# Kernel tuning notes

Hardware: AMD Instinct MI355X
Metric: run time of the kernel (lower is better)

## Reference

```python
import jax, jax.numpy as jnp
import numpy as np

B_, CIN, HH, WW = 2, 64, 64, 64
D_MODEL, D_INNER, D_STATE, DT_RANK, D_CONV = 64, 128, 16, 32, 3


def setup_inputs() -> dict:
    key = jax.random.key(0)
    ks = jax.random.split(key, 16)
    w = lambda k, shape: jax.random.normal(k, shape, jnp.float32) * 0.05
    # dt_proj bias init (torch: inv-softplus of dt sampled in [dt_min, dt_max])
    dt = jnp.exp(jax.random.uniform(ks[10], (D_INNER,)) * (np.log(0.1) - np.log(0.001)) + np.log(0.001))
    dt = jnp.clip(dt, 1e-4, None)
    inv_dt = dt + jnp.log(-jnp.expm1(-dt))
    A = jnp.tile(jnp.arange(1, D_STATE + 1, dtype=jnp.float32), (D_INNER, 1))
    return {
        "rgb_feat": jax.random.normal(ks[0], (B_, CIN, HH, WW), jnp.float32),
        "dte_feat": jax.random.normal(ks[1], (B_, CIN, HH, WW), jnp.float32),
        "conv1_w": w(ks[2], (D_MODEL, CIN)), "conv1_b": jnp.zeros((D_MODEL,), jnp.float32),
        "conv2_w": w(ks[3], (D_MODEL, CIN)), "conv2_b": jnp.zeros((D_MODEL,), jnp.float32),
        "conv3_w": w(ks[4], (CIN, D_MODEL)), "conv3_b": jnp.zeros((CIN,), jnp.float32),
        "norm_w": jnp.ones((D_MODEL,), jnp.float32),
        "in_proj_w": w(ks[5], (2 * D_INNER, D_MODEL)),
        "conv1d_w": w(ks[6], (D_INNER, D_CONV)), "conv1d_b": jnp.zeros((D_INNER,), jnp.float32),
        "x_proj_w": w(ks[7], (DT_RANK + 2 * D_STATE, D_INNER)),
        "dt_proj_w": jax.random.uniform(ks[8], (D_INNER, DT_RANK), jnp.float32, -DT_RANK ** -0.5, DT_RANK ** -0.5),
        "dt_proj_b": inv_dt,
        "A_log": jnp.log(A),
        "Dp": jnp.ones((D_INNER,), jnp.float32),
        "out_proj_w": w(ks[9], (D_MODEL, D_INNER)),
    }


def _conv1x1(x, w, b):
    return jnp.einsum('bchw,oc->bohw', x, w) + b[None, :, None, None]


def _rmsnorm(x, w, eps=1e-5):
    return x * jax.lax.rsqrt(jnp.mean(x * x, axis=-1, keepdims=True) + eps) * w


def _dwconv1d(x, w, b):
    # x: [B,L,D]; depthwise conv, kernel 3, padding 1 (same length)
    xt = jnp.transpose(x, (0, 2, 1))  # [B,D,L]
    y = jax.lax.conv_general_dilated(xt, w[:, None, :], (1,), [(1, 1)],
                                     dimension_numbers=('NCH', 'OIH', 'NCH'),
                                     feature_group_count=D_INNER)
    return jnp.transpose(y + b[None, :, None], (0, 2, 1))


def _mamba(x, h, p):
    # x: [B,L,d_model]
    xz = x @ p['in_proj_w'].T                      # [B,L,2*d_inner]
    xc, z = jnp.split(xz, 2, axis=-1)
    xc = jax.nn.silu(_dwconv1d(xc, p['conv1d_w'], p['conv1d_b']))
    A = -jnp.exp(p['A_log'])                       # [D,S]
    dbc = xc @ p['x_proj_w'].T                     # [B,L,dt_rank+2S]
    delta, Bm, Cm = jnp.split(dbc, [DT_RANK, DT_RANK + D_STATE], axis=-1)
    delta = jax.nn.softplus(delta @ p['dt_proj_w'].T + p['dt_proj_b'])  # [B,L,D]
    deltaA = jnp.exp(delta[..., None] * A)         # [B,L,D,S]
    BX = delta[..., None] * Bm[:, :, None, :] * xc[..., None]  # [B,L,D,S]
    h = deltaA * h + BX
    y = jnp.einsum('blds,bls->bld', h, Cm) + p['Dp'] * xc
    out = (y * jax.nn.silu(z)) @ p['out_proj_w'].T
    return out, h


def _residual_block(x4d, h, p):
    B, C, H, W = x4d.shape
    x = jnp.transpose(x4d.reshape(B, C, H * W), (0, 2, 1))  # [B,L,C]
    x = _rmsnorm(x, p['norm_w'])
    out, h = _mamba(x, h, p)
    out = out + x
    return jnp.transpose(out, (0, 2, 1)).reshape(B, C, H, W), h


def _rsfm(rgb_feat, dte_feat, conv1_w, conv1_b, conv2_w, conv2_b, conv3_w, conv3_b,
          norm_w, in_proj_w, conv1d_w, conv1d_b, x_proj_w, dt_proj_w, dt_proj_b,
          A_log, Dp, out_proj_w):
    p = dict(norm_w=norm_w, in_proj_w=in_proj_w, conv1d_w=conv1d_w, conv1d_b=conv1d_b,
             x_proj_w=x_proj_w, dt_proj_w=dt_proj_w, dt_proj_b=dt_proj_b,
             A_log=A_log, Dp=Dp, out_proj_w=out_proj_w)
    rgb = _conv1x1(rgb_feat, conv1_w, conv1_b)
    dte = _conv1x1(dte_feat, conv2_w, conv2_b)
    B = rgb.shape[0]
    h = jnp.zeros((B, HH * WW, D_INNER, D_STATE), jnp.float32)
    out1, h = _residual_block(rgb, h, p)
    out2, h = _residual_block(dte + out1, h, p)
    out3, h = _residual_block(rgb + out2, h, p)
    out4, h = _residual_block(dte + out3, h, p)
    out5, h = _residual_block(rgb + out4, h, p)
    out6, h = _residual_block(dte + out5, h, p)
    return _conv1x1(out6, conv3_w, conv3_b), h


def reference(rgb_feat, dte_feat, conv1_w, conv1_b, conv2_w, conv2_b, conv3_w, conv3_b,
              norm_w, in_proj_w, conv1d_w, conv1d_b, x_proj_w, dt_proj_w, dt_proj_b,
              A_log, Dp, out_proj_w):
    return _rsfm(rgb_feat, dte_feat, conv1_w, conv1_b, conv2_w, conv2_b, conv3_w, conv3_b,
                 norm_w, in_proj_w, conv1d_w, conv1d_b, x_proj_w, dt_proj_w, dt_proj_b,
                 A_log, Dp, out_proj_w)
```

## Files before the change

kernel.cpp:

```cpp
#include <hip/hip_runtime.h>

typedef unsigned short u16;
typedef unsigned int u32;

#define LSEQ 4096
#define NPOS 8192

__device__ __forceinline__ float bf2f(u16 u){
  union { u32 i; float f; } v; v.i = ((u32)u) << 16; return v.f;
}
__device__ __forceinline__ u16 f2bf(float f){
  union { float f; u32 i; } v; v.f = f;
  u32 x = v.i;
  return (u16)((x + 0x7fffu + ((x >> 16) & 1u)) >> 16);
}
__device__ __forceinline__ float2 up2(u32 u){
  union { u32 i; float f; } a, b;
  a.i = u << 16; b.i = u & 0xffff0000u;
  float2 r; r.x = a.f; r.y = b.f; return r;
}
__device__ __forceinline__ u32 pk2(float a, float b){
  return (u32)f2bf(a) | ((u32)f2bf(b) << 16);
}
__device__ __forceinline__ float silu_f(float x){ return x / (1.f + __expf(-x)); }
__device__ __forceinline__ float softplus_f(float x){
  return fmaxf(x, 0.f) + log1pf(__expf(-fabsf(x)));
}

__global__ __launch_bounds__(256) void k_prep(
    const float* __restrict__ ipw, const float* __restrict__ xpw,
    const float* __restrict__ dtw, const float* __restrict__ opw,
    const float* __restrict__ w1, const float* __restrict__ w2,
    const float* __restrict__ w3, const float* __restrict__ alog,
    float* __restrict__ ipT, float* __restrict__ xpT,
    float* __restrict__ dtT, float* __restrict__ opT,
    float* __restrict__ w1T, float* __restrict__ w2T,
    float* __restrict__ w3T, float* __restrict__ Aneg)
{
  int t = blockIdx.x * 256 + threadIdx.x;
  if (t < 16384){ int o = t >> 6, c = t & 63; ipT[c * 256 + o] = ipw[t]; }
  if (t < 8192){ int o = t >> 7, d = t & 127; xpT[d * 64 + o] = xpw[t]; }
  if (t < 4096){ int d = t >> 5, r = t & 31; dtT[r * 128 + d] = dtw[t]; }
  if (t < 8192){ int o = t >> 7, d = t & 127; opT[d * 64 + o] = opw[t]; }
  if (t < 4096){ int o = t >> 6, c = t & 63;
                 w1T[c*64+o] = w1[t]; w2T[c*64+o] = w2[t]; w3T[c*64+o] = w3[t]; }
  if (t < 2048){ Aneg[t] = -__expf(alog[t]); }
}

__global__ __launch_bounds__(256) void k_convin(
    const float* __restrict__ rgb, const float* __restrict__ dte,
    const float* __restrict__ w1T, const float* __restrict__ b1,
    const float* __restrict__ w2T, const float* __restrict__ b2,
    float* __restrict__ rgbp, float* __restrict__ dtep)
{
  __shared__ __align__(16) float xt[64][64];
  __shared__ __align__(16) float ot[64][65];
  const int tid = threadIdx.x;
  const int which = blockIdx.x & 1;
  const int n0 = (blockIdx.x >> 1) * 64;
  const int b = n0 >> 12, l0 = n0 & 4095;
  const float* src = which ? dte : rgb;
  const float* wT  = which ? w2T : w1T;
  const float* bb  = which ? b2 : b1;
  float* o = which ? dtep : rgbp;

  #pragma unroll
  for (int j = 0; j < 16; j++){
    int idx = tid + 256 * j;
    int c = idx >> 6, p = idx & 63;
    xt[c][p] = src[(size_t)b * 262144 + (size_t)c * 4096 + l0 + p];
  }
  __syncthreads();

  const int pos = tid & 63;
  const int cb  = (tid >> 6) * 16;
  float acc[16];
  #pragma unroll
  for (int j = 0; j < 16; j++) acc[j] = bb[cb + j];
  for (int c = 0; c < 64; c++){
    float xv = xt[c][pos];
    #pragma unroll
    for (int j = 0; j < 16; j++) acc[j] += wT[c*64 + cb + j] * xv;
  }
  #pragma unroll
  for (int j = 0; j < 16; j++) ot[pos][cb + j] = acc[j];
  __syncthreads();
  #pragma unroll
  for (int j = 0; j < 16; j++){
    int idx = tid + 256 * j;
    int p = idx >> 6, c = idx & 63;
    o[(size_t)(n0 + p)*64 + c] = ot[p][c];
  }
}

__global__ __launch_bounds__(256) void k_pre(
    const float* __restrict__ xin, const float* __restrict__ normw,
    const float* __restrict__ ipT,
    float* __restrict__ xn, float* __restrict__ xcp, float* __restrict__ zs)
{
  __shared__ __align__(16) float xnl[4][2][64];
  const int wv = threadIdx.x >> 6, lane = threadIdx.x & 63;
  const int n0 = (blockIdx.x * 4 + wv) * 2;
  float nw = normw[lane];
  #pragma unroll
  for (int p = 0; p < 2; p++){
    int n = n0 + p;
    float v = xin[(size_t)n*64 + lane];
    float ss = v * v;
    for (int m = 32; m > 0; m >>= 1) ss += __shfl_xor(ss, m);
    v = v * rsqrtf(ss * (1.f/64.f) + 1e-5f) * nw;
    xn[(size_t)n*64 + lane] = v;
    xnl[wv][p][lane] = v;
  }
  float ac[2][4] = {};
  for (int c = 0; c < 64; c++){
    float w0 = ipT[c*256 + lane],       w1 = ipT[c*256 + 64 + lane];
    float w2 = ipT[c*256 + 128 + lane], w3 = ipT[c*256 + 192 + lane];
    #pragma unroll
    for (int p = 0; p < 2; p++){
      float xv = xnl[wv][p][c];
      ac[p][0] += w0*xv; ac[p][1] += w1*xv; ac[p][2] += w2*xv; ac[p][3] += w3*xv;
    }
  }
  #pragma unroll
  for (int p = 0; p < 2; p++){
    int n = n0 + p;
    xcp[(size_t)n*128 + lane]      = ac[p][0];
    xcp[(size_t)n*128 + 64 + lane] = ac[p][1];
    zs[(size_t)n*128 + lane]       = silu_f(ac[p][2]);
    zs[(size_t)n*128 + 64 + lane]  = silu_f(ac[p][3]);
  }
}

__global__ __launch_bounds__(256) void k_step(
    const float* __restrict__ xcpA, float* __restrict__ xcpB,
    float* __restrict__ zs, float* __restrict__ xn,
    u16* __restrict__ hbf, float* __restrict__ hfin,
    const float* __restrict__ base_next,
    const float* __restrict__ xpT, const float* __restrict__ dtT,
    const float* __restrict__ opT, const float* __restrict__ Aneg,
    const float* __restrict__ c1w, const float* __restrict__ c1b,
    const float* __restrict__ dtb, const float* __restrict__ Dpw,
    const float* __restrict__ normw, const float* __restrict__ ipT,
    int hasH, int fusePre)
{
  __shared__ __align__(16) float xcl[4][2][128];
  __shared__ __align__(16) float dbl[4][2][64];
  __shared__ __align__(16) float yzl[4][2][128];
  __shared__ __align__(16) float xnl[4][2][64];
  const int wv = threadIdx.x >> 6, lane = threadIdx.x & 63;
  const int n0 = (blockIdx.x * 4 + wv) * 2;
  const int d0 = lane, d1 = 64 + lane;

  float cw00 = c1w[d0*3+0], cw01 = c1w[d0*3+1], cw02 = c1w[d0*3+2];
  float cw10 = c1w[d1*3+0], cw11 = c1w[d1*3+1], cw12 = c1w[d1*3+2];
  float cb0 = c1b[d0], cb1 = c1b[d1];

  float xc0[2], xc1[2];
  #pragma unroll
  for (int p = 0; p < 2; p++){
    int n = n0 + p, l = n & 4095;
    const float* xr = xcpA + (size_t)n * 128;
    float am0 = 0.f, am1 = 0.f, ap0 = 0.f, ap1 = 0.f;
    if (l > 0)    { am0 = xr[d0 - 128]; am1 = xr[d1 - 128]; }
    float a00 = xr[d0], a01 = xr[d1];
    if (l < 4095) { ap0 = xr[d0 + 128]; ap1 = xr[d1 + 128]; }
    float v0 = silu_f(cw00*am0 + cw01*a00 + cw02*ap0 + cb0);
    float v1 = silu_f(cw10*am1 + cw11*a01 + cw12*ap1 + cb1);
    xc0[p] = v0; xc1[p] = v1;
    xcl[wv][p][d0] = v0; xcl[wv][p][d1] = v1;
  }

  {
    float xa[2] = {0,0};
    for (int d = 0; d < 128; d++){
      float w = xpT[d*64 + lane];
      #pragma unroll
      for (int p = 0; p < 2; p++) xa[p] += w * xcl[wv][p][d];
    }
    #pragma unroll
    for (int p = 0; p < 2; p++) dbl[wv][p][lane] = xa[p];
  }

  float dl0[2], dl1[2];
  {
    float tb0 = dtb[d0], tb1 = dtb[d1];
    float da0[2] = {tb0, tb0}, da1[2] = {tb1, tb1};
    for (int r = 0; r < 32; r++){
      float w0 = dtT[r*128 + d0], w1 = dtT[r*128 + d1];
      #pragma unroll
      for (int p = 0; p < 2; p++){
        float bv = dbl[wv][p][r];
        da0[p] += w0 * bv; da1[p] += w1 * bv;
      }
    }
    #pragma unroll
    for (int p = 0; p < 2; p++){ dl0[p] = softplus_f(da0[p]); dl1[p] = softplus_f(da1[p]); }
  }

  float an0[16], an1[16];
  {
    const float4* A0 = (const float4*)(Aneg + d0*16);
    const float4* A1 = (const float4*)(Aneg + d1*16);
    #pragma unroll
    for (int q = 0; q < 4; q++){
      float4 a = A0[q]; an0[q*4+0]=a.x; an0[q*4+1]=a.y; an0[q*4+2]=a.z; an0[q*4+3]=a.w;
      float4 b = A1[q]; an1[q*4+0]=b.x; an1[q*4+1]=b.y; an1[q*4+2]=b.z; an1[q*4+3]=b.w;
    }
  }
  float dp0 = Dpw[d0], dp1 = Dpw[d1];

  #pragma unroll 1
  for (int p = 0; p < 2; p++){
    int n = n0 + p;
    float Bm[16], Cm[16];
    {
      const float4* bb = (const float4*)&dbl[wv][p][32];
      const float4* cc = (const float4*)&dbl[wv][p][48];
      #pragma unroll
      for (int q = 0; q < 4; q++){
        float4 a = bb[q]; Bm[q*4+0]=a.x; Bm[q*4+1]=a.y; Bm[q*4+2]=a.z; Bm[q*4+3]=a.w;
        float4 b = cc[q]; Cm[q*4+0]=b.x; Cm[q*4+1]=b.y; Cm[q*4+2]=b.z; Cm[q*4+3]=b.w;
      }
    }
    u16* hp0 = hbf + ((size_t)n*2048 + (size_t)d0*16);
    u16* hp1 = hbf + ((size_t)n*2048 + (size_t)d1*16);
    float h0[16], h1[16];
    if (hasH){
      #pragma unroll
      for (int q = 0; q < 2; q++){
        uint4 v = ((const uint4*)hp0)[q];
        float2 t0=up2(v.x), t1=up2(v.y), t2=up2(v.z), t3=up2(v.w);
        h0[q*8+0]=t0.x; h0[q*8+1]=t0.y; h0[q*8+2]=t1.x; h0[q*8+3]=t1.y;
        h0[q*8+4]=t2.x; h0[q*8+5]=t2.y; h0[q*8+6]=t3.x; h0[q*8+7]=t3.y;
        uint4 w = ((const uint4*)hp1)[q];
        float2 s0=up2(w.x), s1=up2(w.y), s2=up2(w.z), s3=up2(w.w);
        h1[q*8+0]=s0.x; h1[q*8+1]=s0.y; h1[q*8+2]=s1.x; h1[q*8+3]=s1.y;
        h1[q*8+4]=s2.x; h1[q*8+5]=s2.y; h1[q*8+6]=s3.x; h1[q*8+7]=s3.y;
      }
    } else {
      #pragma unroll
      for (int s = 0; s < 16; s++){ h0[s]=0.f; h1[s]=0.f; }
    }
    float y0 = 0.f, y1 = 0.f;
    float bx0 = dl0[p] * xc0[p], bx1 = dl1[p] * xc1[p];
    #pragma unroll
    for (int s = 0; s < 16; s++){
      h0[s] = __expf(dl0[p]*an0[s])*h0[s] + bx0*Bm[s];
      y0 = fmaf(h0[s], Cm[s], y0);
      h1[s] = __expf(dl1[p]*an1[s])*h1[s] + bx1*Bm[s];
      y1 = fmaf(h1[s], Cm[s], y1);
    }
    if (fusePre){
      #pragma unroll
      for (int q = 0; q < 2; q++){
        uint4 v;
        v.x = pk2(h0[q*8+0], h0[q*8+1]); v.y = pk2(h0[q*8+2], h0[q*8+3]);
        v.z = pk2(h0[q*8+4], h0[q*8+5]); v.w = pk2(h0[q*8+6], h0[q*8+7]);
        ((uint4*)hp0)[q] = v;
        uint4 w;
        w.x = pk2(h1[q*8+0], h1[q*8+1]); w.y = pk2(h1[q*8+2], h1[q*8+3]);
        w.z = pk2(h1[q*8+4], h1[q*8+5]); w.w = pk2(h1[q*8+6], h1[q*8+7]);
        ((uint4*)hp1)[q] = w;
      }
    } else {
      float4* f0 = (float4*)(hfin + (size_t)n*2048 + (size_t)d0*16);
      float4* f1 = (float4*)(hfin + (size_t)n*2048 + (size_t)d1*16);
      #pragma unroll
      for (int q = 0; q < 4; q++){
        float4 v; v.x=h0[q*4+0]; v.y=h0[q*4+1]; v.z=h0[q*4+2]; v.w=h0[q*4+3];
        f0[q] = v;
        float4 w; w.x=h1[q*4+0]; w.y=h1[q*4+1]; w.z=h1[q*4+2]; w.w=h1[q*4+3];
        f1[q] = w;
      }
    }
    y0 += dp0 * xc0[p];
    y1 += dp1 * xc1[p];
    yzl[wv][p][d0] = y0 * zs[(size_t)n*128 + d0];
    yzl[wv][p][d1] = y1 * zs[(size_t)n*128 + d1];
  }

  float oa[2] = {0,0};
  for (int d = 0; d < 128; d++){
    float w = opT[d*64 + lane];
    #pragma unroll
    for (int p = 0; p < 2; p++) oa[p] += w * yzl[wv][p][d];
  }

  float nw = normw[lane];
  if (fusePre){
    #pragma unroll
    for (int p = 0; p < 2; p++){
      int n = n0 + p;
      float v = oa[p] + xn[(size_t)n*64 + lane] + base_next[(size_t)n*64 + lane];
      float ss = v * v;
      for (int m = 32; m > 0; m >>= 1) ss += __shfl_xor(ss, m);
      v = v * rsqrtf(ss * (1.f/64.f) + 1e-5f) * nw;
      xn[(size_t)n*64 + lane] = v;
      xnl[wv][p][lane] = v;
    }
    float ac[2][4] = {};
    for (int c = 0; c < 64; c++){
      float w0 = ipT[c*256 + lane],       w1 = ipT[c*256 + 64 + lane];
      float w2 = ipT[c*256 + 128 + lane], w3 = ipT[c*256 + 192 + lane];
      #pragma unroll
      for (int p = 0; p < 2; p++){
        float xv = xnl[wv][p][c];
        ac[p][0] += w0*xv; ac[p][1] += w1*xv; ac[p][2] += w2*xv; ac[p][3] += w3*xv;
      }
    }
    #pragma unroll
    for (int p = 0; p < 2; p++){
      int n = n0 + p;
      xcpB[(size_t)n*128 + lane]      = ac[p][0];
      xcpB[(size_t)n*128 + 64 + lane] = ac[p][1];
      zs[(size_t)n*128 + lane]        = silu_f(ac[p][2]);
      zs[(size_t)n*128 + 64 + lane]   = silu_f(ac[p][3]);
    }
  } else {
    #pragma unroll
    for (int p = 0; p < 2; p++){
      int n = n0 + p;
      xcpB[(size_t)n*64 + lane] = oa[p] + xn[(size_t)n*64 + lane];
    }
  }
}

__global__ __launch_bounds__(256) void k_conv3(
    const float* __restrict__ out6, const float* __restrict__ w3T,
    const float* __restrict__ b3, float* __restrict__ out)
{
  __shared__ __align__(16) float t[64][65];
  const int tid = threadIdx.x;
  const int n0 = blockIdx.x * 64;
  #pragma unroll
  for (int i = 0; i < 16; i++){
    int idx = tid + 256*i;
    int r = idx >> 6, c = idx & 63;
    t[r][c] = out6[(size_t)(n0 + r)*64 + c];
  }
  __syncthreads();
  const int i = tid & 63;
  const int cb = (tid >> 6) * 16;
  float acc[16];
  #pragma unroll
  for (int j = 0; j < 16; j++) acc[j] = b3[cb + j];
  for (int o = 0; o < 64; o++){
    float xv = t[i][o];
    #pragma unroll
    for (int j = 0; j < 16; j++) acc[j] += w3T[o*64 + cb + j] * xv;
  }
  const int b = n0 >> 12;
  const int l = (n0 & 4095) + i;
  #pragma unroll
  for (int j = 0; j < 16; j++)
    out[(size_t)b*262144 + (size_t)(cb + j)*4096 + l] = acc[j];
}

extern "C" void kernel_launch(void* const* d_in, const int* in_sizes, int n_in,
                              void* d_out, int out_size, void* d_ws, size_t ws_size,
                              hipStream_t stream)
{
  const float* rgb  = (const float*)d_in[0];
  const float* dte  = (const float*)d_in[1];
  const float* w1   = (const float*)d_in[2];
  const float* b1   = (const float*)d_in[3];
  const float* w2   = (const float*)d_in[4];
  const float* b2   = (const float*)d_in[5];
  const float* w3   = (const float*)d_in[6];
  const float* b3   = (const float*)d_in[7];
  const float* nrm  = (const float*)d_in[8];
  const float* ipw  = (const float*)d_in[9];
  const float* c1w  = (const float*)d_in[10];
  const float* c1b  = (const float*)d_in[11];
  const float* xpw  = (const float*)d_in[12];
  const float* dtw  = (const float*)d_in[13];
  const float* dtb  = (const float*)d_in[14];
  const float* alog = (const float*)d_in[15];
  const float* Dpw  = (const float*)d_in[16];
  const float* opw  = (const float*)d_in[17];

  float* outc = (float*)d_out;
  float* hfin = outc + 524288;

  float* ws   = (float*)d_ws;
  float* xcp0 = ws;
  float* xcp1 = ws + 1048576;
  float* rgbp = ws + 2097152;
  float* dtep = ws + 2621440;
  float* xnb  = ws + 3145728;
  float* zsb  = ws + 3670016;
  float* wb   = ws + 4718592;
  float* ipT  = wb;
  float* xpT  = wb + 16384;
  float* dtT  = wb + 24576;
  float* opT  = wb + 28672;
  float* w1T  = wb + 36864;
  float* w2T  = wb + 40960;
  float* w3T  = wb + 45056;
  float* Aneg = wb + 49152;
  u16*   hbf  = (u16*)(ws + 4769792);

  k_prep<<<64, 256, 0, stream>>>(ipw, xpw, dtw, opw, w1, w2, w3, alog,
                                 ipT, xpT, dtT, opT, w1T, w2T, w3T, Aneg);
  k_convin<<<256, 256, 0, stream>>>(rgb, dte, w1T, b1, w2T, b2, rgbp, dtep);
  k_pre<<<1024, 256, 0, stream>>>(rgbp, nrm, ipT, xnb, xcp0, zsb);

  float* xa[2] = {xcp0, xcp1};
  for (int k = 0; k < 6; k++){
    const float* base = (k == 5) ? rgbp  : ((k & 1) ? rgbp : dtep);
    k_step<<<1024, 256, 0, stream>>>(xa[k & 1], xa[(k & 1) ^ 1], zsb, xnb,
                                     hbf, hfin, base,
                                     xpT, dtT, opT, Aneg, c1w, c1b, dtb, Dpw,
                                     nrm, ipT, (k > 0) ? 1 : 0, (k < 5) ? 1 : 0);
  }
  k_conv3<<<128, 256, 0, stream>>>(xcp0, w3T, b3, outc);
}
```

Measured before the change: 364.4 us.

## Stage bf16-packed projection weights in LDS and broadcast activations via readlane

```diff
diff --git a/kernel.cpp b/kernel.cpp
--- a/kernel.cpp
+++ b/kernel.cpp
@@ -25,6 +25,9 @@
 __device__ __forceinline__ float silu_f(float x){ return x / (1.f + __expf(-x)); }
 __device__ __forceinline__ float softplus_f(float x){
   return fmaxf(x, 0.f) + log1pf(__expf(-fabsf(x)));
+}
+__device__ __forceinline__ float rdl(float v, int l){
+  return __int_as_float(__builtin_amdgcn_readlane(__float_as_int(v), l));
 }
 
 __global__ __launch_bounds__(256) void k_prep(
@@ -32,18 +35,25 @@
     const float* __restrict__ dtw, const float* __restrict__ opw,
     const float* __restrict__ w1, const float* __restrict__ w2,
     const float* __restrict__ w3, const float* __restrict__ alog,
-    float* __restrict__ ipT, float* __restrict__ xpT,
-    float* __restrict__ dtT, float* __restrict__ opT,
-    float* __restrict__ w1T, float* __restrict__ w2T,
-    float* __restrict__ w3T, float* __restrict__ Aneg)
+    u32* __restrict__ ipP, u32* __restrict__ xpP, u32* __restrict__ opP,
+    float* __restrict__ dtT, float* __restrict__ w1T,
+    float* __restrict__ w2T, float* __restrict__ w3T,
+    float* __restrict__ Aneg)
 {
   int t = blockIdx.x * 256 + threadIdx.x;
-  if (t < 16384){ int o = t >> 6, c = t & 63; ipT[c * 256 + o] = ipw[t]; }
-  if (t < 8192){ int o = t >> 7, d = t & 127; xpT[d * 64 + o] = xpw[t]; }
-  if (t < 4096){ int d = t >> 5, r = t & 31; dtT[r * 128 + d] = dtw[t]; }
-  if (t < 8192){ int o = t >> 7, d = t & 127; opT[d * 64 + o] = opw[t]; }
-  if (t < 4096){ int o = t >> 6, c = t & 63;
-                 w1T[c*64+o] = w1[t]; w2T[c*64+o] = w2[t]; w3T[c*64+o] = w3[t]; }
+  if (t < 8192){
+    int c = t >> 7, j = t & 127;
+    ipP[t] = pk2(ipw[j*64 + c], ipw[(j + 128)*64 + c]);
+  }
+  if (t < 4096){
+    int dd = t >> 6, o = t & 63;
+    xpP[t] = pk2(xpw[o*128 + 2*dd], xpw[o*128 + 2*dd + 1]);
+    opP[t] = pk2(opw[o*128 + 2*dd], opw[o*128 + 2*dd + 1]);
+    int d = t >> 5, r = t & 31;
+    dtT[r*128 + d] = dtw[t];
+    int o2 = t >> 6, c2 = t & 63;
+    w1T[c2*64 + o2] = w1[t]; w2T[c2*64 + o2] = w2[t]; w3T[c2*64 + o2] = w3[t];
+  }
   if (t < 2048){ Aneg[t] = -__expf(alog[t]); }
 }
 
@@ -93,68 +103,92 @@
   }
 }
 
-__global__ __launch_bounds__(256) void k_pre(
+__global__ __launch_bounds__(512) void k_pre(
     const float* __restrict__ xin, const float* __restrict__ normw,
-    const float* __restrict__ ipT,
+    const u32* __restrict__ wpk,
     float* __restrict__ xn, float* __restrict__ xcp, float* __restrict__ zs)
 {
-  __shared__ __align__(16) float xnl[4][2][64];
-  const int wv = threadIdx.x >> 6, lane = threadIdx.x & 63;
-  const int n0 = (blockIdx.x * 4 + wv) * 2;
+  __shared__ u32 ipS[8192];
+  const int tid = threadIdx.x;
+  #pragma unroll
+  for (int j = 0; j < 4; j++)
+    ((uint4*)ipS)[tid + 512*j] = ((const uint4*)wpk)[tid + 512*j];
+  __syncthreads();
+
+  const int wv = tid >> 6, lane = tid & 63;
+  const int n0 = (blockIdx.x * 8 + wv) * 2;
   float nw = normw[lane];
+  float v[2];
   #pragma unroll
   for (int p = 0; p < 2; p++){
     int n = n0 + p;
-    float v = xin[(size_t)n*64 + lane];
-    float ss = v * v;
+    float x = xin[(size_t)n*64 + lane];
+    float ss = x * x;
     for (int m = 32; m > 0; m >>= 1) ss += __shfl_xor(ss, m);
-    v = v * rsqrtf(ss * (1.f/64.f) + 1e-5f) * nw;
-    xn[(size_t)n*64 + lane] = v;
-    xnl[wv][p][lane] = v;
-  }
-  float ac[2][4] = {};
+    x = x * rsqrtf(ss * (1.f/64.f) + 1e-5f) * nw;
+    v[p] = x;
+    xn[(size_t)n*64 + lane] = x;
+  }
+  float ax0[2] = {0,0}, ax1[2] = {0,0}, az0[2] = {0,0}, az1[2] = {0,0};
+  #pragma unroll
   for (int c = 0; c < 64; c++){
-    float w0 = ipT[c*256 + lane],       w1 = ipT[c*256 + 64 + lane];
-    float w2 = ipT[c*256 + 128 + lane], w3 = ipT[c*256 + 192 + lane];
-    #pragma unroll
-    for (int p = 0; p < 2; p++){
-      float xv = xnl[wv][p][c];
-      ac[p][0] += w0*xv; ac[p][1] += w1*xv; ac[p][2] += w2*xv; ac[p][3] += w3*xv;
+    float2 wa = up2(ipS[c*128 + lane]);
+    float2 wb = up2(ipS[c*128 + 64 + lane]);
+    #pragma unroll
+    for (int p = 0; p < 2; p++){
+      float xv = rdl(v[p], c);
+      ax0[p] += wa.x * xv; az0[p] += wa.y * xv;
+      ax1[p] += wb.x * xv; az1[p] += wb.y * xv;
     }
   }
   #pragma unroll
   for (int p = 0; p < 2; p++){
     int n = n0 + p;
-    xcp[(size_t)n*128 + lane]      = ac[p][0];
-    xcp[(size_t)n*128 + 64 + lane] = ac[p][1];
-    zs[(size_t)n*128 + lane]       = silu_f(ac[p][2]);
-    zs[(size_t)n*128 + 64 + lane]  = silu_f(ac[p][3]);
-  }
-}
-
-__global__ __launch_bounds__(256) void k_step(
+    xcp[(size_t)n*128 + lane]      = ax0[p];
+    xcp[(size_t)n*128 + 64 + lane] = ax1[p];
+    zs[(size_t)n*128 + lane]       = silu_f(az0[p]);
+    zs[(size_t)n*128 + 64 + lane]  = silu_f(az1[p]);
+  }
+}
+
+__global__ __launch_bounds__(512, 4) void k_step(
     const float* __restrict__ xcpA, float* __restrict__ xcpB,
     float* __restrict__ zs, float* __restrict__ xn,
     u16* __restrict__ hbf, float* __restrict__ hfin,
-    const float* __restrict__ base_next,
-    const float* __restrict__ xpT, const float* __restrict__ dtT,
-    const float* __restrict__ opT, const float* __restrict__ Aneg,
+    const float* __restrict__ base_next, const u32* __restrict__ wpk,
+    const float* __restrict__ dtT, const float* __restrict__ Aneg,
     const float* __restrict__ c1w, const float* __restrict__ c1b,
     const float* __restrict__ dtb, const float* __restrict__ Dpw,
-    const float* __restrict__ normw, const float* __restrict__ ipT,
-    int hasH, int fusePre)
-{
-  __shared__ __align__(16) float xcl[4][2][128];
-  __shared__ __align__(16) float dbl[4][2][64];
-  __shared__ __align__(16) float yzl[4][2][128];
-  __shared__ __align__(16) float xnl[4][2][64];
-  const int wv = threadIdx.x >> 6, lane = threadIdx.x & 63;
-  const int n0 = (blockIdx.x * 4 + wv) * 2;
+    const float* __restrict__ normw, int hasH, int fusePre)
+{
+  __shared__ u32 wS[16384];
+  const int tid = threadIdx.x;
+  #pragma unroll
+  for (int j = 0; j < 8; j++)
+    ((uint4*)wS)[tid + 512*j] = ((const uint4*)wpk)[tid + 512*j];
+  const u32* ipS = wS;
+  const u32* xpS = wS + 8192;
+  const u32* opS = wS + 12288;
+  __syncthreads();
+
+  const int wv = tid >> 6, lane = tid & 63;
+  const int n0 = (blockIdx.x * 8 + wv) * 2;
   const int d0 = lane, d1 = 64 + lane;
 
-  float cw00 = c1w[d0*3+0], cw01 = c1w[d0*3+1], cw02 = c1w[d0*3+2];
-  float cw10 = c1w[d1*3+0], cw11 = c1w[d1*3+1], cw12 = c1w[d1*3+2];
-  float cb0 = c1b[d0], cb1 = c1b[d1];
+  uint4 hr0[2][2], hr1[2][2];
+  if (hasH){
+    #pragma unroll
+    for (int p = 0; p < 2; p++){
+      const uint4* q0 = (const uint4*)(hbf + ((size_t)(n0+p)*2048 + (size_t)d0*16));
+      const uint4* q1 = (const uint4*)(hbf + ((size_t)(n0+p)*2048 + (size_t)d1*16));
+      hr0[p][0] = q0[0]; hr0[p][1] = q0[1];
+      hr1[p][0] = q1[0]; hr1[p][1] = q1[1];
+    }
+  }
+
+  const float cw00 = c1w[d0*3+0], cw01 = c1w[d0*3+1], cw02 = c1w[d0*3+2];
+  const float cw10 = c1w[d1*3+0], cw11 = c1w[d1*3+1], cw12 = c1w[d1*3+2];
+  const float cb0 = c1b[d0], cb1 = c1b[d1];
 
   float xc0[2], xc1[2];
   #pragma unroll
@@ -165,37 +199,43 @@
     if (l > 0)    { am0 = xr[d0 - 128]; am1 = xr[d1 - 128]; }
     float a00 = xr[d0], a01 = xr[d1];
     if (l < 4095) { ap0 = xr[d0 + 128]; ap1 = xr[d1 + 128]; }
-    float v0 = silu_f(cw00*am0 + cw01*a00 + cw02*ap0 + cb0);
-    float v1 = silu_f(cw10*am1 + cw11*a01 + cw12*ap1 + cb1);
-    xc0[p] = v0; xc1[p] = v1;
-    xcl[wv][p][d0] = v0; xcl[wv][p][d1] = v1;
-  }
-
-  {
-    float xa[2] = {0,0};
-    for (int d = 0; d < 128; d++){
-      float w = xpT[d*64 + lane];
-      #pragma unroll
-      for (int p = 0; p < 2; p++) xa[p] += w * xcl[wv][p][d];
-    }
-    #pragma unroll
-    for (int p = 0; p < 2; p++) dbl[wv][p][lane] = xa[p];
+    xc0[p] = silu_f(cw00*am0 + cw01*a00 + cw02*ap0 + cb0);
+    xc1[p] = silu_f(cw10*am1 + cw11*a01 + cw12*ap1 + cb1);
+  }
+
+  float xa[2] = {0.f, 0.f};
+  #pragma unroll
+  for (int dd = 0; dd < 32; dd++){
+    float2 w = up2(xpS[dd*64 + lane]);
+    #pragma unroll
+    for (int p = 0; p < 2; p++)
+      xa[p] += w.x * rdl(xc0[p], 2*dd) + w.y * rdl(xc0[p], 2*dd + 1);
+  }
+  #pragma unroll
+  for (int dd = 32; dd < 64; dd++){
+    float2 w = up2(xpS[dd*64 + lane]);
+    #pragma unroll
+    for (int p = 0; p < 2; p++)
+      xa[p] += w.x * rdl(xc1[p], 2*dd - 64) + w.y * rdl(xc1[p], 2*dd - 63);
   }
 
   float dl0[2], dl1[2];
   {
     float tb0 = dtb[d0], tb1 = dtb[d1];
     float da0[2] = {tb0, tb0}, da1[2] = {tb1, tb1};
+    #pragma unroll
     for (int r = 0; r < 32; r++){
       float w0 = dtT[r*128 + d0], w1 = dtT[r*128 + d1];
       #pragma unroll
       for (int p = 0; p < 2; p++){
-        float bv = dbl[wv][p][r];
+        float bv = rdl(xa[p], r);
         da0[p] += w0 * bv; da1[p] += w1 * bv;
       }
     }
     #pragma unroll
-    for (int p = 0; p < 2; p++){ dl0[p] = softplus_f(da0[p]); dl1[p] = softplus_f(da1[p]); }
+    for (int p = 0; p < 2; p++){
+      dl0[p] = softplus_f(da0[p]); dl1[p] = softplus_f(da1[p]);
+    }
   }
 
   float an0[16], an1[16];
@@ -208,60 +248,53 @@
       float4 b = A1[q]; an1[q*4+0]=b.x; an1[q*4+1]=b.y; an1[q*4+2]=b.z; an1[q*4+3]=b.w;
     }
   }
-  float dp0 = Dpw[d0], dp1 = Dpw[d1];
-
-  #pragma unroll 1
+  const float dp0 = Dpw[d0], dp1 = Dpw[d1];
+
+  float yz0[2], yz1[2];
+  #pragma unroll
   for (int p = 0; p < 2; p++){
     int n = n0 + p;
-    float Bm[16], Cm[16];
-    {
-      const float4* bb = (const float4*)&dbl[wv][p][32];
-      const float4* cc = (const float4*)&dbl[wv][p][48];
-      #pragma unroll
-      for (int q = 0; q < 4; q++){
-        float4 a = bb[q]; Bm[q*4+0]=a.x; Bm[q*4+1]=a.y; Bm[q*4+2]=a.z; Bm[q*4+3]=a.w;
-        float4 b = cc[q]; Cm[q*4+0]=b.x; Cm[q*4+1]=b.y; Cm[q*4+2]=b.z; Cm[q*4+3]=b.w;
-      }
-    }
-    u16* hp0 = hbf + ((size_t)n*2048 + (size_t)d0*16);
-    u16* hp1 = hbf + ((size_t)n*2048 + (size_t)d1*16);
     float h0[16], h1[16];
     if (hasH){
       #pragma unroll
       for (int q = 0; q < 2; q++){
-        uint4 v = ((const uint4*)hp0)[q];
-        float2 t0=up2(v.x), t1=up2(v.y), t2=up2(v.z), t3=up2(v.w);
+        float2 t0 = up2(hr0[p][q].x), t1 = up2(hr0[p][q].y);
+        float2 t2 = up2(hr0[p][q].z), t3 = up2(hr0[p][q].w);
         h0[q*8+0]=t0.x; h0[q*8+1]=t0.y; h0[q*8+2]=t1.x; h0[q*8+3]=t1.y;
         h0[q*8+4]=t2.x; h0[q*8+5]=t2.y; h0[q*8+6]=t3.x; h0[q*8+7]=t3.y;
-        uint4 w = ((const uint4*)hp1)[q];
-        float2 s0=up2(w.x), s1=up2(w.y), s2=up2(w.z), s3=up2(w.w);
+        float2 s0 = up2(hr1[p][q].x), s1 = up2(hr1[p][q].y);
+        float2 s2 = up2(hr1[p][q].z), s3 = up2(hr1[p][q].w);
         h1[q*8+0]=s0.x; h1[q*8+1]=s0.y; h1[q*8+2]=s1.x; h1[q*8+3]=s1.y;
         h1[q*8+4]=s2.x; h1[q*8+5]=s2.y; h1[q*8+6]=s3.x; h1[q*8+7]=s3.y;
       }
     } else {
       #pragma unroll
-      for (int s = 0; s < 16; s++){ h0[s]=0.f; h1[s]=0.f; }
+      for (int s = 0; s < 16; s++){ h0[s] = 0.f; h1[s] = 0.f; }
     }
     float y0 = 0.f, y1 = 0.f;
     float bx0 = dl0[p] * xc0[p], bx1 = dl1[p] * xc1[p];
     #pragma unroll
     for (int s = 0; s < 16; s++){
-      h0[s] = __expf(dl0[p]*an0[s])*h0[s] + bx0*Bm[s];
-      y0 = fmaf(h0[s], Cm[s], y0);
-      h1[s] = __expf(dl1[p]*an1[s])*h1[s] + bx1*Bm[s];
-      y1 = fmaf(h1[s], Cm[s], y1);
+      float Bs = rdl(xa[p], 32 + s);
+      float Cs = rdl(xa[p], 48 + s);
+      h0[s] = __expf(dl0[p]*an0[s])*h0[s] + bx0*Bs;
+      y0 = fmaf(h0[s], Cs, y0);
+      h1[s] = __expf(dl1[p]*an1[s])*h1[s] + bx1*Bs;
+      y1 = fmaf(h1[s], Cs, y1);
     }
     if (fusePre){
+      u16* o0 = hbf + ((size_t)n*2048 + (size_t)d0*16);
+      u16* o1 = hbf + ((size_t)n*2048 + (size_t)d1*16);
       #pragma unroll
       for (int q = 0; q < 2; q++){
         uint4 v;
         v.x = pk2(h0[q*8+0], h0[q*8+1]); v.y = pk2(h0[q*8+2], h0[q*8+3]);
         v.z = pk2(h0[q*8+4], h0[q*8+5]); v.w = pk2(h0[q*8+6], h0[q*8+7]);
-        ((uint4*)hp0)[q] = v;
+        ((uint4*)o0)[q] = v;
         uint4 w;
         w.x = pk2(h1[q*8+0], h1[q*8+1]); w.y = pk2(h1[q*8+2], h1[q*8+3]);
         w.z = pk2(h1[q*8+4], h1[q*8+5]); w.w = pk2(h1[q*8+6], h1[q*8+7]);
-        ((uint4*)hp1)[q] = w;
+        ((uint4*)o1)[q] = w;
       }
     } else {
       float4* f0 = (float4*)(hfin + (size_t)n*2048 + (size_t)d0*16);
@@ -274,48 +307,58 @@
         f1[q] = w;
       }
     }
-    y0 += dp0 * xc0[p];
-    y1 += dp1 * xc1[p];
-    yzl[wv][p][d0] = y0 * zs[(size_t)n*128 + d0];
-    yzl[wv][p][d1] = y1 * zs[(size_t)n*128 + d1];
-  }
-
-  float oa[2] = {0,0};
-  for (int d = 0; d < 128; d++){
-    float w = opT[d*64 + lane];
-    #pragma unroll
-    for (int p = 0; p < 2; p++) oa[p] += w * yzl[wv][p][d];
-  }
-
-  float nw = normw[lane];
+    yz0[p] = (y0 + dp0 * xc0[p]) * zs[(size_t)n*128 + lane];
+    yz1[p] = (y1 + dp1 * xc1[p]) * zs[(size_t)n*128 + 64 + lane];
+  }
+
+  float oa[2] = {0.f, 0.f};
+  #pragma unroll
+  for (int dd = 0; dd < 32; dd++){
+    float2 w = up2(opS[dd*64 + lane]);
+    #pragma unroll
+    for (int p = 0; p < 2; p++)
+      oa[p] += w.x * rdl(yz0[p], 2*dd) + w.y * rdl(yz0[p], 2*dd + 1);
+  }
+  #pragma unroll
+  for (int dd = 32; dd < 64; dd++){
+    float2 w = up2(opS[dd*64 + lane]);
+    #pragma unroll
+    for (int p = 0; p < 2; p++)
+      oa[p] += w.x * rdl(yz1[p], 2*dd - 64) + w.y * rdl(yz1[p], 2*dd - 63);
+  }
+
+  const float nw = normw[lane];
   if (fusePre){
+    float v[2];
     #pragma unroll
     for (int p = 0; p < 2; p++){
       int n = n0 + p;
-      float v = oa[p] + xn[(size_t)n*64 + lane] + base_next[(size_t)n*64 + lane];
-      float ss = v * v;
+      float x = oa[p] + xn[(size_t)n*64 + lane] + base_next[(size_t)n*64 + lane];
+      float ss = x * x;
       for (int m = 32; m > 0; m >>= 1) ss += __shfl_xor(ss, m);
-      v = v * rsqrtf(ss * (1.f/64.f) + 1e-5f) * nw;
-      xn[(size_t)n*64 + lane] = v;
-      xnl[wv][p][lane] = v;
-    }
-    float ac[2][4] = {};
+      x = x * rsqrtf(ss * (1.f/64.f) + 1e-5f) * nw;
+      v[p] = x;
+      xn[(size_t)n*64 + lane] = x;
+    }
+    float ax0[2] = {0,0}, ax1[2] = {0,0}, az0[2] = {0,0}, az1[2] = {0,0};
+    #pragma unroll
     for (int c = 0; c < 64; c++){
-      float w0 = ipT[c*256 + lane],       w1 = ipT[c*256 + 64 + lane];
-      float w2 = ipT[c*256 + 128 + lane], w3 = ipT[c*256 + 192 + lane];
+      float2 wa = up2(ipS[c*128 + lane]);
+      float2 wb = up2(ipS[c*128 + 64 + lane]);
       #pragma unroll
       for (int p = 0; p < 2; p++){
-        float xv = xnl[wv][p][c];
-        ac[p][0] += w0*xv; ac[p][1] += w1*xv; ac[p][2] += w2*xv; ac[p][3] += w3*xv;
+        float xv = rdl(v[p], c);
+        ax0[p] += wa.x * xv; az0[p] += wa.y * xv;
+        ax1[p] += wb.x * xv; az1[p] += wb.y * xv;
       }
     }
     #pragma unroll
     for (int p = 0; p < 2; p++){
       int n = n0 + p;
-      xcpB[(size_t)n*128 + lane]      = ac[p][0];
-      xcpB[(size_t)n*128 + 64 + lane] = ac[p][1];
-      zs[(size_t)n*128 + lane]        = silu_f(ac[p][2]);
-      zs[(size_t)n*128 + 64 + lane]   = silu_f(ac[p][3]);
+      xcpB[(size_t)n*128 + lane]      = ax0[p];
+      xcpB[(size_t)n*128 + 64 + lane] = ax1[p];
+      zs[(size_t)n*128 + lane]        = silu_f(az0[p]);
+      zs[(size_t)n*128 + 64 + lane]   = silu_f(az1[p]);
     }
   } else {
     #pragma unroll
@@ -390,29 +433,27 @@
   float* dtep = ws + 2621440;
   float* xnb  = ws + 3145728;
   float* zsb  = ws + 3670016;
-  float* wb   = ws + 4718592;
-  float* ipT  = wb;
-  float* xpT  = wb + 16384;
-  float* dtT  = wb + 24576;
-  float* opT  = wb + 28672;
-  float* w1T  = wb + 36864;
-  float* w2T  = wb + 40960;
-  float* w3T  = wb + 45056;
-  float* Aneg = wb + 49152;
-  u16*   hbf  = (u16*)(ws + 4769792);
+  u32*   wpk  = (u32*)(ws + 4718592);
+  float* dtT  = ws + 4734976;
+  float* w1T  = ws + 4739072;
+  float* w2T  = ws + 4743168;
+  float* w3T  = ws + 4747264;
+  float* Aneg = ws + 4751360;
+  u16*   hbf  = (u16*)(ws + 4753408);
 
   k_prep<<<64, 256, 0, stream>>>(ipw, xpw, dtw, opw, w1, w2, w3, alog,
-                                 ipT, xpT, dtT, opT, w1T, w2T, w3T, Aneg);
+                                 wpk, wpk + 8192, wpk + 12288,
+                                 dtT, w1T, w2T, w3T, Aneg);
   k_convin<<<256, 256, 0, stream>>>(rgb, dte, w1T, b1, w2T, b2, rgbp, dtep);
-  k_pre<<<1024, 256, 0, stream>>>(rgbp, nrm, ipT, xnb, xcp0, zsb);
+  k_pre<<<512, 512, 0, stream>>>(rgbp, nrm, wpk, xnb, xcp0, zsb);
 
   float* xa[2] = {xcp0, xcp1};
   for (int k = 0; k < 6; k++){
-    const float* base = (k == 5) ? rgbp  : ((k & 1) ? rgbp : dtep);
-    k_step<<<1024, 256, 0, stream>>>(xa[k & 1], xa[(k & 1) ^ 1], zsb, xnb,
-                                     hbf, hfin, base,
-                                     xpT, dtT, opT, Aneg, c1w, c1b, dtb, Dpw,
-                                     nrm, ipT, (k > 0) ? 1 : 0, (k < 5) ? 1 : 0);
+    const float* base = (k & 1) ? rgbp : dtep;
+    k_step<<<512, 512, 0, stream>>>(xa[k & 1], xa[(k & 1) ^ 1], zsb, xnb,
+                                    hbf, hfin, base, wpk,
+                                    dtT, Aneg, c1w, c1b, dtb, Dpw, nrm,
+                                    (k > 0) ? 1 : 0, (k < 5) ? 1 : 0);
   }
   k_conv3<<<128, 256, 0, stream>>>(xcp0, w3T, b3, outc);
 }
```

Result: slower. 527.8 us (+44.8%).
